# Performance work log

Hardware: AMD Instinct MI355X
Metric: run time of the kernel (lower is better)

The kernel has to match this reference:

```python
import jax, jax.numpy as jnp
import numpy as np

B, S, D, H = 2, 2048, 2048, 16
HD = D // H
WHERE_CONST = -10000.0

def setup_inputs() -> dict:
    key = jax.random.key(0)
    k1, k2, k3 = jax.random.split(key, 3)
    x = jax.random.normal(k1, (B, S, D), dtype=jnp.float32)
    attention_mask = jnp.zeros((B, 1, 1, S), dtype=jnp.float32)
    w_qkv = jax.random.normal(k2, (D, 3 * D), dtype=jnp.float32) * (1.0 / np.sqrt(D))
    b_qkv = jnp.zeros((3 * D,), dtype=jnp.float32)
    w_dense = jax.random.normal(k3, (D, D), dtype=jnp.float32) * (1.0 / np.sqrt(D))
    b_dense = jnp.zeros((D,), dtype=jnp.float32)
    return {"x": x, "attention_mask": attention_mask, "w_qkv": w_qkv,
            "b_qkv": b_qkv, "w_dense": w_dense, "b_dense": b_dense}

def reference(x, attention_mask, w_qkv, b_qkv, w_dense, b_dense):
    # fused QKV projection: [B,S,3D]
    qkv = jnp.einsum('bsd,de->bse', x, w_qkv) + b_qkv
    # [B,S,H,3*hd] -> [B,H,S,3*hd]
    qkv = qkv.reshape(B, S, H, 3 * HD).transpose(0, 2, 1, 3)
    q, k, v = jnp.split(qkv, 3, axis=-1)  # each [B,H,S,hd]
    # scores [B,H,S,S], scaled
    scores = jnp.einsum('bhqd,bhkd->bhqk', q, k) / np.sqrt(HD)
    causal = jnp.tril(jnp.ones((S, S), dtype=bool))[None, None]
    scores = jnp.where(causal, scores, WHERE_CONST)
    scores = scores + attention_mask
    probs = jax.nn.softmax(scores, axis=-1)
    # attention dropout is identity in eval mode
    ctx = jnp.einsum('bhqk,bhkd->bhqd', probs, v)  # [B,H,S,hd]
    ctx = ctx.transpose(0, 2, 1, 3).reshape(B, S, D)
    out = jnp.einsum('bsd,de->bse', ctx, w_dense) + b_dense
    # output dropout is identity in eval mode
    return out
```

## Files before the change

### kernel.cpp

```cpp
#include <hip/hip_runtime.h>
#include <hip/hip_bf16.h>

typedef __bf16 bf16x8 __attribute__((ext_vector_type(8)));
typedef float f32x4 __attribute__((ext_vector_type(4)));
typedef float f32x16 __attribute__((ext_vector_type(16)));
typedef unsigned short u16;

#define S_ 2048
#define D_ 2048
#define H_ 16
#define HD_ 128
#define SCALE_ 0.08838834764831845f

__device__ __forceinline__ u16 f2bf(float f) {
  unsigned u = __builtin_bit_cast(unsigned, f);
  u += 0x7fffu + ((u >> 16) & 1u);
  return (u16)(u >> 16);
}

__device__ __forceinline__ void gload16(void* lds, const void* g) {
  __builtin_amdgcn_global_load_lds((const __attribute__((address_space(1))) void*)g,
                                   (__attribute__((address_space(3))) void*)lds, 16, 0, 0);
}

__device__ __forceinline__ f32x4 mfma16(bf16x8 a, bf16x8 b, f32x4 c) {
  return __builtin_amdgcn_mfma_f32_16x16x32_bf16(a, b, c, 0, 0, 0);
}
__device__ __forceinline__ f32x16 mfma32(bf16x8 a, bf16x8 b, f32x16 c) {
  return __builtin_amdgcn_mfma_f32_32x32x16_bf16(a, b, c, 0, 0, 0);
}

__device__ __forceinline__ unsigned cvt_pk_bf16(float lo, float hi) {
  unsigned r;
  asm("v_cvt_pk_bf16_f32 %0, %1, %2" : "=v"(r) : "v"(lo), "v"(hi));
  return r;
}

__global__ void k_cast_bf16(const float* __restrict__ in, u16* __restrict__ out, int n4) {
  int i = blockIdx.x * blockDim.x + threadIdx.x;
  if (i < n4) {
    float4 v = ((const float4*)in)[i];
    ushort4 o;
    o.x = f2bf(v.x); o.y = f2bf(v.y); o.z = f2bf(v.z); o.w = f2bf(v.w);
    ((ushort4*)out)[i] = o;
  }
}

__global__ void k_transpose_cast(const float* __restrict__ in, u16* __restrict__ out,
                                 int rows, int cols) {
  __shared__ u16 tile[32][33];
  int c0 = blockIdx.x * 32, r0 = blockIdx.y * 32;
  int tx = threadIdx.x, ty = threadIdx.y;
#pragma unroll
  for (int i = 0; i < 4; i++) {
    int r = r0 + ty + i * 8;
    tile[ty + i * 8][tx] = f2bf(in[(long)r * cols + c0 + tx]);
  }
  __syncthreads();
#pragma unroll
  for (int i = 0; i < 4; i++) {
    int c = c0 + ty + i * 8;
    out[(long)c * rows + r0 + tx] = tile[tx][ty + i * 8];
  }
}

__device__ __forceinline__ void qkv_store(u16* __restrict__ qb, u16* __restrict__ kpk,
                                          u16* __restrict__ vpk, int row, int col, float val) {
  u16 o = f2bf(val);
  int h = col / 384;
  int m3 = col - h * 384;
  int b = row >> 11, s = row & 2047;
  int bh = b * 16 + h, t = s >> 5;
  if (m3 < 128) {
    qb[(long)row * 2048 + h * 128 + m3] = o;
  } else if (m3 < 256) {
    int dd = m3 - 128;
    long idx = ((((long)bh * 64 + t) * 8 + (dd >> 4)) * 64 + (((dd >> 3) & 1) << 5) + (s & 31)) * 8 + (dd & 7);
    kpk[idx] = o;
  } else {
    int dd = m3 - 256;
    long idx = ((((long)bh * 64 + t) * 8 + (((s >> 4) & 1) << 2) + (dd >> 5)) * 64 + (((s >> 3) & 1) << 5) + (dd & 31)) * 8 + (s & 7);
    vpk[idx] = o;
  }
}

template <int MODE>
__global__ __launch_bounds__(256, 2) void k_gemm(const u16* __restrict__ A,
                                                 const u16* __restrict__ Bt,
                                                 const float* __restrict__ bias,
                                                 void* __restrict__ Cv,
                                                 int M, int N, int K, int NTM,
                                                 u16* __restrict__ qb,
                                                 u16* __restrict__ kpk,
                                                 u16* __restrict__ vpk) {
  __shared__ __align__(16) u16 lA[2][128 * 64];
  __shared__ __align__(16) u16 lB[2][128 * 64];
  const int tid = threadIdx.x, w = tid >> 6, l = tid & 63;
  const int wm = w >> 1, wn = w & 1, lr = l & 15, lg = l >> 4;
  const int nwg = NTM * (N >> 7);
  const int per = nwg >> 3;
  const int wgid = ((int)blockIdx.x & 7) * per + ((int)blockIdx.x >> 3);
  const int tm = (wgid % NTM) << 7;
  const int tn = (wgid / NTM) << 7;
  const int NT = K >> 6;

  f32x4 acc[4][4];
#pragma unroll
  for (int m = 0; m < 4; m++)
#pragma unroll
    for (int n = 0; n < 4; n++) acc[m][n] = {0.f, 0.f, 0.f, 0.f};

  auto stageA = [&](int buf, int kt) {
#pragma unroll
    for (int i = 0; i < 4; i++) {
      int base = i * 256 + w * 64;
      int f = base + l, r = f >> 3, cg = (f & 7) ^ (r & 7);
      gload16(&lA[buf][base * 8], &A[(long)(tm + r) * K + kt * 64 + cg * 8]);
    }
  };
  auto stageB = [&](int buf, int kt) {
#pragma unroll
    for (int i = 0; i < 4; i++) {
      int base = i * 256 + w * 64;
      int f = base + l, r = f >> 3, cg = (f & 7) ^ (r & 7);
      gload16(&lB[buf][base * 8], &Bt[(long)(tn + r) * K + kt * 64 + cg * 8]);
    }
  };

  stageA(0, 0);
  stageB(0, 0);
  if (NT > 1) stageA(1, 1);
  asm volatile("s_waitcnt vmcnt(4)" ::: "memory");
  __builtin_amdgcn_s_barrier();

  for (int kt = 0; kt < NT; ++kt) {
    const int b = kt & 1;
    bf16x8 af[4][2], bfr[2][2];
#pragma unroll
    for (int m = 0; m < 4; m++)
#pragma unroll
      for (int k = 0; k < 2; k++) {
        int r = wm * 64 + m * 16 + lr;
        af[m][k] = *(const bf16x8*)&lA[b][r * 64 + ((((k << 2) + lg) ^ (r & 7)) << 3)];
      }
#pragma unroll
    for (int n = 0; n < 2; n++)
#pragma unroll
      for (int k = 0; k < 2; k++) {
        int r = wn * 64 + n * 16 + lr;
        bfr[n][k] = *(const bf16x8*)&lB[b][r * 64 + ((((k << 2) + lg) ^ (r & 7)) << 3)];
      }
    if (kt + 1 < NT) stageB(b ^ 1, kt + 1);
    __builtin_amdgcn_s_barrier();
    asm volatile("s_waitcnt lgkmcnt(0)" ::: "memory");
    __builtin_amdgcn_sched_barrier(0);
    __builtin_amdgcn_s_setprio(1);
#pragma unroll
    for (int m = 0; m < 4; m++)
#pragma unroll
      for (int n = 0; n < 2; n++)
#pragma unroll
        for (int k = 0; k < 2; k++)
          acc[m][n] = mfma16(af[m][k], bfr[n][k], acc[m][n]);
    __builtin_amdgcn_s_setprio(0);
    __builtin_amdgcn_s_barrier();

#pragma unroll
    for (int n = 0; n < 2; n++)
#pragma unroll
      for (int k = 0; k < 2; k++) {
        int r = wn * 64 + (n + 2) * 16 + lr;
        bfr[n][k] = *(const bf16x8*)&lB[b][r * 64 + ((((k << 2) + lg) ^ (r & 7)) << 3)];
      }
    if (kt + 2 < NT) stageA(b, kt + 2);
    __builtin_amdgcn_s_barrier();
    if (kt + 2 < NT)
      asm volatile("s_waitcnt vmcnt(4) lgkmcnt(0)" ::: "memory");
    else
      asm volatile("s_waitcnt vmcnt(0) lgkmcnt(0)" ::: "memory");
    __builtin_amdgcn_sched_barrier(0);
    __builtin_amdgcn_s_setprio(1);
#pragma unroll
    for (int m = 0; m < 4; m++)
#pragma unroll
      for (int n = 0; n < 2; n++)
#pragma unroll
        for (int k = 0; k < 2; k++)
          acc[m][n + 2] = mfma16(af[m][k], bfr[n][k], acc[m][n + 2]);
    __builtin_amdgcn_s_setprio(0);
    __builtin_amdgcn_s_barrier();
  }

#pragma unroll
  for (int n = 0; n < 4; n++) {
    int col = tn + wn * 64 + n * 16 + lr;
    float bv = bias[col];
#pragma unroll
    for (int m = 0; m < 4; m++) {
      int row0 = tm + wm * 64 + m * 16 + lg * 4;
#pragma unroll
      for (int j = 0; j < 4; j++) {
        float v = acc[m][n][j] + bv;
        if constexpr (MODE == 2)
          qkv_store(qb, kpk, vpk, row0 + j, col, v);
        else
          ((float*)Cv)[(long)(row0 + j) * N + col] = v;
      }
    }
  }
}

__global__ __launch_bounds__(256, 2) void k_attn(const u16* __restrict__ qb,
                                                 const u16* __restrict__ kpk,
                                                 const u16* __restrict__ vpk,
                                                 const float* __restrict__ amask,
                                                 u16* __restrict__ ctx) {
  const int bh = blockIdx.x, b = bh >> 4, h = bh & 15;
  const int tid = threadIdx.x, w = tid >> 6, l = tid & 63;
  const int lr5 = l & 31, hi = l >> 5;
  const int p = blockIdx.y * 4 + w;

  const u16* kbase = kpk + (long)bh * 64 * 8 * 512 + l * 8;
  const u16* vbase = vpk + (long)bh * 64 * 8 * 512 + l * 8;
  const float* ab0 = amask + b * S_;

  auto process = [&](int c) {
    const int qrow0 = c << 5;
    const int nt = c + 1;

    bf16x8 qf[8];
    {
      const u16* qp = qb + (long)(b * S_ + qrow0 + lr5) * 2048 + h * HD_ + hi * 8;
#pragma unroll
      for (int ks = 0; ks < 8; ks++) qf[ks] = *(const bf16x8*)(qp + ks * 16);
    }

    f32x16 aO[4];
#pragma unroll
    for (int db = 0; db < 4; db++)
#pragma unroll
      for (int r = 0; r < 16; r++) aO[db][r] = 0.f;
    float mrun = -3.0e38f, lrun = 0.f;

    bf16x8 kA[8], kB[8];
#pragma unroll
    for (int f = 0; f < 8; f++) kA[f] = *(const bf16x8*)(kbase + f * 512);

    auto body = [&](bf16x8 (&cur)[8], bf16x8 (&nxt)[8], int t) {
      const int t32 = t << 5;
      bf16x8 vf[8];
      {
        const u16* vp = vbase + (long)t * 4096;
#pragma unroll
        for (int f = 0; f < 8; f++) vf[f] = *(const bf16x8*)(vp + f * 512);
      }
      f32x4 am[4];
#pragma unroll
      for (int rg = 0; rg < 4; rg++) am[rg] = *(const f32x4*)(ab0 + t32 + rg * 8 + hi * 4);

      f32x16 aS;
#pragma unroll
      for (int r = 0; r < 16; r++) aS[r] = 0.f;
      __builtin_amdgcn_s_setprio(1);
#pragma unroll
      for (int ks = 0; ks < 8; ks++) aS = mfma32(cur[ks], qf[ks], aS);
      __builtin_amdgcn_s_setprio(0);

      if (t + 1 < nt) {
        const u16* kp = kbase + (long)(t + 1) * 4096;
#pragma unroll
        for (int f = 0; f < 8; f++) nxt[f] = *(const bf16x8*)(kp + f * 512);
      }

      float v[16];
      const bool needmask = (t == c);
#pragma unroll
      for (int rg = 0; rg < 4; rg++)
#pragma unroll
        for (int j = 0; j < 4; j++) {
          v[rg * 4 + j] = fmaf(aS[rg * 4 + j], SCALE_, am[rg][j]);
          if (needmask && (rg * 8 + hi * 4 + j > lr5)) v[rg * 4 + j] = -1e30f;
        }
      float mx = v[0];
#pragma unroll
      for (int i = 1; i < 16; i++) mx = fmaxf(mx, v[i]);
      mx = fmaxf(mx, __shfl_xor(mx, 32));

      if (!__all(mx <= mrun + 8.0f)) {
        float mnew = fmaxf(mrun, mx);
        float corr = __expf(mrun - mnew);
        lrun *= corr;
        mrun = mnew;
#pragma unroll
        for (int reg = 0; reg < 16; reg++) {
          float cb = __shfl(corr, (reg & 3) + 8 * (reg >> 2) + 4 * hi);
#pragma unroll
          for (int db = 0; db < 4; db++) aO[db][reg] *= cb;
        }
      }

      float ls = 0.f;
#pragma unroll
      for (int i = 0; i < 16; i++) { v[i] = __expf(v[i] - mrun); ls += v[i]; }
      ls += __shfl_xor(ls, 32);
      lrun += ls;

      unsigned pk[8];
#pragma unroll
      for (int q = 0; q < 8; q++) pk[q] = cvt_pk_bf16(v[2 * q], v[2 * q + 1]);
      bf16x8 pa[2];
#pragma unroll
      for (int kst = 0; kst < 2; kst++) {
        unsigned a0 = pk[4 * kst], a1 = pk[4 * kst + 1], a2 = pk[4 * kst + 2], a3 = pk[4 * kst + 3];
        unsigned s0 = hi ? a0 : a2;
        unsigned s1 = hi ? a1 : a3;
        unsigned r0 = __shfl_xor(s0, 32);
        unsigned r1 = __shfl_xor(s1, 32);
        union { unsigned u[4]; bf16x8 vv; } U;
        U.u[0] = hi ? r0 : a0;
        U.u[1] = hi ? r1 : a1;
        U.u[2] = hi ? a2 : r0;
        U.u[3] = hi ? a3 : r1;
        pa[kst] = U.vv;
      }

      __builtin_amdgcn_s_setprio(1);
#pragma unroll
      for (int kst = 0; kst < 2; kst++)
#pragma unroll
        for (int db = 0; db < 4; db++)
          aO[db] = mfma32(pa[kst], vf[kst * 4 + db], aO[db]);
      __builtin_amdgcn_s_setprio(0);
    };

    for (int t = 0; t < nt; t += 2) {
      body(kA, kB, t);
      if (t + 1 < nt) body(kB, kA, t + 1);
    }

    float inv = 1.0f / lrun;
#pragma unroll
    for (int reg = 0; reg < 16; reg++) {
      int r = (reg & 3) + 8 * (reg >> 2) + 4 * hi;
      float ib = __shfl(inv, r);
      int srow = qrow0 + r;
#pragma unroll
      for (int db = 0; db < 4; db++)
        ctx[(long)(b * S_ + srow) * D_ + h * HD_ + db * 32 + lr5] = f2bf(aO[db][reg] * ib);
    }
  };

  process(63 - p);
  process(p);
}

extern "C" void kernel_launch(void* const* d_in, const int* in_sizes, int n_in,
                              void* d_out, int out_size, void* d_ws, size_t ws_size,
                              hipStream_t stream) {
  const float* x  = (const float*)d_in[0];
  const float* am = (const float*)d_in[1];
  const float* wq = (const float*)d_in[2];
  const float* bq = (const float*)d_in[3];
  const float* wd = (const float*)d_in[4];
  const float* bd = (const float*)d_in[5];
  float* out = (float*)d_out;
  char* ws = (char*)d_ws;

  const size_t MB = 1048576;
  u16* xb   = (u16*)(ws);
  u16* wqT  = (u16*)(ws + 16 * MB);
  u16* qb   = (u16*)(ws + 40 * MB);
  u16* kpk  = (u16*)(ws + 56 * MB);
  u16* vpk  = (u16*)(ws + 72 * MB);
  u16* ctxb = (u16*)(ws);
  u16* wdT  = (u16*)(ws + 16 * MB);

  k_cast_bf16<<<8192, 256, 0, stream>>>(x, xb, 2097152);
  k_transpose_cast<<<dim3(192, 64), dim3(32, 8), 0, stream>>>(wq, wqT, 2048, 6144);
  k_gemm<2><<<1536, 256, 0, stream>>>(xb, wqT, bq, nullptr, 4096, 6144, 2048, 32, qb, kpk, vpk);
  k_transpose_cast<<<dim3(64, 64), dim3(32, 8), 0, stream>>>(wd, wdT, 2048, 2048);
  k_attn<<<dim3(32, 8), 256, 0, stream>>>(qb, kpk, vpk, am, ctxb);
  k_gemm<0><<<512, 256, 0, stream>>>(ctxb, wdT, bd, out, 4096, 2048, 2048, 32,
                                     nullptr, nullptr, nullptr);
}
```

Measured before the change: 260.5 us.

## Use exp2 softmax, sync attention waves on shared tiles, vectorize weight transpose

```diff
diff --git a/kernel.cpp b/kernel.cpp
--- a/kernel.cpp
+++ b/kernel.cpp
@@ -11,6 +11,9 @@
 #define H_ 16
 #define HD_ 128
 #define SCALE_ 0.08838834764831845f
+#define SCL2_ 0.12751791939574715f
+#define LOG2E_ 1.4426950408889634f
+#define THR2_ 11.541560327111707f
 
 __device__ __forceinline__ u16 f2bf(float f) {
   unsigned u = __builtin_bit_cast(unsigned, f);
@@ -46,21 +49,35 @@
   }
 }
 
+__global__ void k_scale_mask(const float* __restrict__ in, float* __restrict__ out, int n) {
+  int i = blockIdx.x * blockDim.x + threadIdx.x;
+  if (i < n) out[i] = in[i] * LOG2E_;
+}
+
 __global__ void k_transpose_cast(const float* __restrict__ in, u16* __restrict__ out,
                                  int rows, int cols) {
-  __shared__ u16 tile[32][33];
-  int c0 = blockIdx.x * 32, r0 = blockIdx.y * 32;
-  int tx = threadIdx.x, ty = threadIdx.y;
+  __shared__ u16 tile[64][66];
+  const int c0 = blockIdx.x * 64, r0 = blockIdx.y * 64;
+  const int tx = threadIdx.x & 15, ty = threadIdx.x >> 4;
 #pragma unroll
   for (int i = 0; i < 4; i++) {
-    int r = r0 + ty + i * 8;
-    tile[ty + i * 8][tx] = f2bf(in[(long)r * cols + c0 + tx]);
+    int r = ty + i * 16;
+    float4 v = *(const float4*)&in[(long)(r0 + r) * cols + c0 + tx * 4];
+    tile[r][tx * 4 + 0] = f2bf(v.x);
+    tile[r][tx * 4 + 1] = f2bf(v.y);
+    tile[r][tx * 4 + 2] = f2bf(v.z);
+    tile[r][tx * 4 + 3] = f2bf(v.w);
   }
   __syncthreads();
 #pragma unroll
   for (int i = 0; i < 4; i++) {
-    int c = c0 + ty + i * 8;
-    out[(long)c * rows + r0 + tx] = tile[tx][ty + i * 8];
+    int cc = ty + i * 16;
+    ushort4 o;
+    o.x = tile[tx * 4 + 0][cc];
+    o.y = tile[tx * 4 + 1][cc];
+    o.z = tile[tx * 4 + 2][cc];
+    o.w = tile[tx * 4 + 3][cc];
+    *(ushort4*)&out[(long)(c0 + cc) * rows + r0 + tx * 4] = o;
   }
 }
 
@@ -213,20 +230,20 @@
 __global__ __launch_bounds__(256, 2) void k_attn(const u16* __restrict__ qb,
                                                  const u16* __restrict__ kpk,
                                                  const u16* __restrict__ vpk,
-                                                 const float* __restrict__ amask,
+                                                 const float* __restrict__ amask2,
                                                  u16* __restrict__ ctx) {
   const int bh = blockIdx.x, b = bh >> 4, h = bh & 15;
   const int tid = threadIdx.x, w = tid >> 6, l = tid & 63;
   const int lr5 = l & 31, hi = l >> 5;
-  const int p = blockIdx.y * 4 + w;
+  const int pp = blockIdx.y;
 
   const u16* kbase = kpk + (long)bh * 64 * 8 * 512 + l * 8;
   const u16* vbase = vpk + (long)bh * 64 * 8 * 512 + l * 8;
-  const float* ab0 = amask + b * S_;
-
-  auto process = [&](int c) {
+  const float* ab0 = amask2 + b * S_;
+
+  auto process = [&](int nt_iter, int c) {
     const int qrow0 = c << 5;
-    const int nt = c + 1;
+    const int mynt = c + 1;
 
     bf16x8 qf[8];
     {
@@ -247,6 +264,8 @@
     for (int f = 0; f < 8; f++) kA[f] = *(const bf16x8*)(kbase + f * 512);
 
     auto body = [&](bf16x8 (&cur)[8], bf16x8 (&nxt)[8], int t) {
+      __builtin_amdgcn_s_barrier();
+      if (t >= mynt) return;
       const int t32 = t << 5;
       bf16x8 vf[8];
       {
@@ -266,7 +285,7 @@
       for (int ks = 0; ks < 8; ks++) aS = mfma32(cur[ks], qf[ks], aS);
       __builtin_amdgcn_s_setprio(0);
 
-      if (t + 1 < nt) {
+      if (t + 1 < mynt) {
         const u16* kp = kbase + (long)(t + 1) * 4096;
 #pragma unroll
         for (int f = 0; f < 8; f++) nxt[f] = *(const bf16x8*)(kp + f * 512);
@@ -278,7 +297,7 @@
       for (int rg = 0; rg < 4; rg++)
 #pragma unroll
         for (int j = 0; j < 4; j++) {
-          v[rg * 4 + j] = fmaf(aS[rg * 4 + j], SCALE_, am[rg][j]);
+          v[rg * 4 + j] = fmaf(aS[rg * 4 + j], SCL2_, am[rg][j]);
           if (needmask && (rg * 8 + hi * 4 + j > lr5)) v[rg * 4 + j] = -1e30f;
         }
       float mx = v[0];
@@ -286,9 +305,9 @@
       for (int i = 1; i < 16; i++) mx = fmaxf(mx, v[i]);
       mx = fmaxf(mx, __shfl_xor(mx, 32));
 
-      if (!__all(mx <= mrun + 8.0f)) {
+      if (!__all(mx <= mrun + THR2_)) {
         float mnew = fmaxf(mrun, mx);
-        float corr = __expf(mrun - mnew);
+        float corr = exp2f(mrun - mnew);
         lrun *= corr;
         mrun = mnew;
 #pragma unroll
@@ -301,7 +320,7 @@
 
       float ls = 0.f;
 #pragma unroll
-      for (int i = 0; i < 16; i++) { v[i] = __expf(v[i] - mrun); ls += v[i]; }
+      for (int i = 0; i < 16; i++) { v[i] = exp2f(v[i] - mrun); ls += v[i]; }
       ls += __shfl_xor(ls, 32);
       lrun += ls;
 
@@ -333,9 +352,9 @@
       __builtin_amdgcn_s_setprio(0);
     };
 
-    for (int t = 0; t < nt; t += 2) {
+    for (int t = 0; t < nt_iter; t += 2) {
       body(kA, kB, t);
-      if (t + 1 < nt) body(kB, kA, t + 1);
+      if (t + 1 < nt_iter) body(kB, kA, t + 1);
     }
 
     float inv = 1.0f / lrun;
@@ -350,8 +369,8 @@
     }
   };
 
-  process(63 - p);
-  process(p);
+  process(64 - 4 * pp, 63 - (4 * pp + w));
+  process(4 * pp + 4, 4 * pp + w);
 }
 
 extern "C" void kernel_launch(void* const* d_in, const int* in_sizes, int n_in,
@@ -372,14 +391,16 @@
   u16* qb   = (u16*)(ws + 40 * MB);
   u16* kpk  = (u16*)(ws + 56 * MB);
   u16* vpk  = (u16*)(ws + 72 * MB);
+  float* am2 = (float*)(ws + 88 * MB);
   u16* ctxb = (u16*)(ws);
   u16* wdT  = (u16*)(ws + 16 * MB);
 
   k_cast_bf16<<<8192, 256, 0, stream>>>(x, xb, 2097152);
-  k_transpose_cast<<<dim3(192, 64), dim3(32, 8), 0, stream>>>(wq, wqT, 2048, 6144);
+  k_scale_mask<<<16, 256, 0, stream>>>(am, am2, 4096);
+  k_transpose_cast<<<dim3(96, 32), 256, 0, stream>>>(wq, wqT, 2048, 6144);
   k_gemm<2><<<1536, 256, 0, stream>>>(xb, wqT, bq, nullptr, 4096, 6144, 2048, 32, qb, kpk, vpk);
-  k_transpose_cast<<<dim3(64, 64), dim3(32, 8), 0, stream>>>(wd, wdT, 2048, 2048);
-  k_attn<<<dim3(32, 8), 256, 0, stream>>>(qb, kpk, vpk, am, ctxb);
+  k_transpose_cast<<<dim3(32, 32), 256, 0, stream>>>(wd, wdT, 2048, 2048);
+  k_attn<<<dim3(32, 8), 256, 0, stream>>>(qb, kpk, vpk, am2, ctxb);
   k_gemm<0><<<512, 256, 0, stream>>>(ctxb, wdT, bd, out, 4096, 2048, 2048, 32,
                                      nullptr, nullptr, nullptr);
 }
```

After: 289.6 us. 1.11x slower.
